# Optimization experiments

Hardware: AMD Instinct MI355X
Metric: run time of the kernel (lower is better)

## Reference

```python
import jax, jax.numpy as jnp
import numpy as np

EPS = 1e-3  # Keras BatchNormalization default epsilon
HEADS = 4
KEY_DEPTH = 16   # k
INTRA = 1        # u
VAL_DEPTH = 64   # v = kernel_out // heads = 256 // 4
C_IN = 256
B, HH, WW = 16, 32, 32
N = HH * WW      # == size of positional embedding


def setup_inputs() -> dict:
    key = jax.random.key(0)
    ks = jax.random.split(key, 6)
    x = jax.random.normal(ks[0], (B, HH, WW, C_IN), dtype=jnp.float32)
    # 1x1 conv kernels == dense matrices over the channel dim
    Wq = jax.random.normal(ks[1], (C_IN, KEY_DEPTH * HEADS), dtype=jnp.float32) * 0.05
    Wk = jax.random.normal(ks[2], (C_IN, KEY_DEPTH * INTRA), dtype=jnp.float32) * 0.05
    Wv = jax.random.normal(ks[3], (C_IN, VAL_DEPTH * INTRA), dtype=jnp.float32) * 0.05
    # BatchNorm (inference mode) parameters
    gamma_q = jnp.ones((KEY_DEPTH * HEADS,), jnp.float32)
    beta_q = jnp.zeros((KEY_DEPTH * HEADS,), jnp.float32)
    mean_q = jnp.zeros((KEY_DEPTH * HEADS,), jnp.float32)
    var_q = jnp.ones((KEY_DEPTH * HEADS,), jnp.float32)
    gamma_v = jnp.ones((VAL_DEPTH * INTRA,), jnp.float32)
    beta_v = jnp.zeros((VAL_DEPTH * INTRA,), jnp.float32)
    mean_v = jnp.zeros((VAL_DEPTH * INTRA,), jnp.float32)
    var_v = jnp.ones((VAL_DEPTH * INTRA,), jnp.float32)
    # Positional embedding: [size, size, key_depth, intra_depth], uniform init
    E = jax.random.uniform(ks[4], (N, N, KEY_DEPTH, INTRA), dtype=jnp.float32)
    return {
        'x': x, 'Wq': Wq, 'Wk': Wk, 'Wv': Wv,
        'gamma_q': gamma_q, 'beta_q': beta_q, 'mean_q': mean_q, 'var_q': var_q,
        'gamma_v': gamma_v, 'beta_v': beta_v, 'mean_v': mean_v, 'var_v': var_v,
        'E': E,
    }


def _bn(t, gamma, beta, mean, var):
    return gamma * (t - mean) / jnp.sqrt(var + EPS) + beta


def reference(x, Wq, Wk, Wv, gamma_q, beta_q, mean_q, var_q,
              gamma_v, beta_v, mean_v, var_v, E):
    b, hh, ww, _ = x.shape
    n = hh * ww
    # 1x1 conv projections (context c == x)
    q = jnp.einsum('bhwc,cd->bhwd', x, Wq)           # [b,hh,ww,h*k]
    k = jnp.einsum('bhwc,cd->bhwd', x, Wk)           # [b,hh,ww,u*k]
    v = jnp.einsum('bhwc,cd->bhwd', x, Wv)           # [b,hh,ww,u*v]
    q = _bn(q, gamma_q, beta_q, mean_q, var_q)
    v = _bn(v, gamma_v, beta_v, mean_v, var_v)
    # softmax over the channel axis (faithful to the source code)
    k = jax.nn.softmax(k, axis=-1)
    # rearranges: b hh ww (h k) -> b h k n ; b hh ww (u k) -> b u k n ; b hh ww (u v) -> b u v n
    q = q.reshape(b, n, HEADS, KEY_DEPTH).transpose(0, 2, 3, 1)   # [b,h,k,n]
    k = k.reshape(b, n, INTRA, KEY_DEPTH).transpose(0, 2, 3, 1)   # [b,u,k,n]
    v = v.reshape(b, n, INTRA, VAL_DEPTH).transpose(0, 2, 3, 1)   # [b,u,v,n]
    # content lambda: sum over intra-depth and positions
    lam_c = jnp.einsum('bukn,buvn->bkv', k, v)                    # [b,k,v]
    Yc = jnp.einsum('bhkn,bkv->bhvn', q, lam_c)                   # [b,h,v,n]
    # positional lambdas: E[n,m,k,u] contracted with v[b,u,v,m]
    lam_p = jnp.einsum('nmku,buvm->bnkv', E, v)                   # [b,n,k,v]
    Yp = jnp.einsum('bhkn,bnkv->bhvn', q, lam_p)                  # [b,h,v,n]
    Y = Yc + Yp                                                    # [b,h,v,n]
    # b h v n -> b hh ww (h v)
    out = Y.transpose(0, 3, 1, 2).reshape(b, hh, ww, HEADS * VAL_DEPTH)
    return out
```

## Files before the change

kernel.cpp:

```cpp
#include <hip/hip_runtime.h>
#include <stdint.h>

#define EPS 1e-3f

typedef __bf16 bf16x8 __attribute__((ext_vector_type(8)));
typedef float  f32x4  __attribute__((ext_vector_type(4)));

static __device__ __forceinline__ uint16_t f2bf(float f) {
  union { float f; uint32_t u; } v; v.f = f;
  uint32_t u = v.u;
  uint32_t r = u + 0x7fffu + ((u >> 16) & 1u);
  return (uint16_t)(r >> 16);
}
static __device__ __forceinline__ void gload_lds16(const void* g, void* l) {
  __builtin_amdgcn_global_load_lds(
      (const __attribute__((address_space(1))) unsigned int*)g,
      (__attribute__((address_space(3))) unsigned int*)l, 16, 0, 0);
}

__global__ __launch_bounds__(256) void econv(
    const float* __restrict__ E, uint16_t* __restrict__ Ebf,
    const float* __restrict__ Wq, const float* __restrict__ Wk,
    const float* __restrict__ Wv, uint16_t* __restrict__ WtP)
{
  const int n = blockIdx.x, t = threadIdx.x;
  if (n < 144) {
    const int col = n;
    float val = (col < 64) ? Wq[t * 64 + col]
              : (col < 80) ? Wk[t * 16 + (col - 64)]
                           : Wv[t * 64 + (col - 80)];
    WtP[col * 264 + t] = f2bf(val);
  }
  const float* En = E + (size_t)n * 16384;
#pragma unroll 1
  for (int kq = 0; kq < 4; ++kq) {
#pragma unroll
    for (int mi = 0; mi < 4; ++mi) {
      int m = mi * 256 + t;
      float4 d = *(const float4*)&En[m * 16 + kq * 4];
      const float* dp = (const float*)&d;
#pragma unroll
      for (int j = 0; j < 4; ++j) {
        int k = kq * 4 + j;
        Ebf[(size_t)(n * 16 + k) * 1024 + m] = f2bf(dp[j]);
      }
    }
  }
}

__global__ __launch_bounds__(256) void proj_mfma(
    const float* __restrict__ x, const uint16_t* __restrict__ WtP,
    const float* __restrict__ gq, const float* __restrict__ bq,
    const float* __restrict__ mq, const float* __restrict__ vq,
    const float* __restrict__ gv, const float* __restrict__ bv,
    const float* __restrict__ mv, const float* __restrict__ vvp,
    float* __restrict__ Qf, uint16_t* __restrict__ VbfT,
    float* __restrict__ part)
{
  __shared__ __align__(16) char smem[111616];
  uint16_t* const xA = (uint16_t*)smem;
  char* const Wt = smem + 33792;

  const int t = threadIdx.x;
  const int wid = t >> 6, lane = t & 63;
  const int bid = blockIdx.x;
  const int b = bid >> 4, mc = bid & 15;
  const int r0 = b * 1024 + mc * 64;

#pragma unroll
  for (int i = 0; i < 19; ++i) {
    int off = (i * 256 + t) * 16;
    gload_lds16((const char*)WtP + off, Wt + off);
  }
  {
    const int row = t >> 2, ks0 = (t & 3) * 64;
    const float* src = x + (size_t)(r0 + row) * 256 + ks0;
    uint16_t* dstp = xA + row * 264 + ks0;
#pragma unroll
    for (int i = 0; i < 8; ++i) {
      float4 d0 = *(const float4*)(src + i * 8);
      float4 d1 = *(const float4*)(src + i * 8 + 4);
      union { uint16_t u[8]; uint4 q; } pk;
      pk.u[0] = f2bf(d0.x); pk.u[1] = f2bf(d0.y);
      pk.u[2] = f2bf(d0.z); pk.u[3] = f2bf(d0.w);
      pk.u[4] = f2bf(d1.x); pk.u[5] = f2bf(d1.y);
      pk.u[6] = f2bf(d1.z); pk.u[7] = f2bf(d1.w);
      *(uint4*)(dstp + i * 8) = pk.q;
    }
  }
  __syncthreads();

  f32x4 acc[9];
#pragma unroll
  for (int f = 0; f < 9; ++f) acc[f] = f32x4{0.f, 0.f, 0.f, 0.f};
  const int arow = wid * 16 + (lane & 15);
#pragma unroll
  for (int kst = 0; kst < 8; ++kst) {
    const int sb = kst * 64 + ((lane >> 4) << 4);
    bf16x8 af = *(const bf16x8*)((const char*)xA + arow * 528 + sb);
#pragma unroll
    for (int f = 0; f < 9; ++f) {
      const int crow = f * 16 + (lane & 15);
      bf16x8 bfr = *(const bf16x8*)(Wt + crow * 528 + sb);
      acc[f] = __builtin_amdgcn_mfma_f32_16x16x32_bf16(af, bfr, acc[f], 0, 0, 0);
    }
  }

  const int cl = lane & 15;
  const int rbase = wid * 16 + ((lane >> 4) << 2);

  float qs[4], qb[4], qm[4], vs[4], vb[4], vm[4];
#pragma unroll
  for (int f = 0; f < 4; ++f) {
    const int c = f * 16 + cl;
    qs[f] = gq[c] * rsqrtf(vq[c] + EPS); qb[f] = bq[c]; qm[f] = mq[c];
    vs[f] = gv[c] * rsqrtf(vvp[c] + EPS); vb[f] = bv[c]; vm[f] = mv[c];
  }
#pragma unroll
  for (int f = 0; f < 4; ++f)
#pragma unroll
    for (int r = 0; r < 4; ++r)
      Qf[(size_t)(r0 + rbase + r) * 64 + f * 16 + cl] =
          (acc[f][r] - qm[f]) * qs[f] + qb[f];
  float ex[4];
#pragma unroll
  for (int r = 0; r < 4; ++r) {
    float kv = acc[4][r];
    float mx = kv;
#pragma unroll
    for (int d = 1; d < 16; d <<= 1) mx = fmaxf(mx, __shfl_xor(mx, d, 64));
    float e = __expf(kv - mx);
    float sm = e;
#pragma unroll
    for (int d = 1; d < 16; d <<= 1) sm += __shfl_xor(sm, d, 64);
    ex[r] = e / sm;
  }
  float vv[4][4];
#pragma unroll
  for (int f = 0; f < 4; ++f)
#pragma unroll
    for (int r = 0; r < 4; ++r)
      vv[f][r] = (acc[5 + f][r] - vm[f]) * vs[f] + vb[f];

  __syncthreads();
  float* const vt = (float*)smem;
  float* const ks = (float*)(smem + 64 * 65 * 4);
#pragma unroll
  for (int r = 0; r < 4; ++r) ks[(rbase + r) * 20 + cl] = ex[r];
#pragma unroll
  for (int f = 0; f < 4; ++f)
#pragma unroll
    for (int r = 0; r < 4; ++r) vt[(rbase + r) * 65 + f * 16 + cl] = vv[f][r];
  __syncthreads();

  {
    const int v = t & 63, grp = t >> 6;
#pragma unroll
    for (int h = 0; h < 2; ++h) {
      union { uint16_t u16[8]; uint4 q; } pk;
#pragma unroll
      for (int i = 0; i < 8; ++i)
        pk.u16[i] = f2bf(vt[(grp * 16 + h * 8 + i) * 65 + v]);
      *(uint4*)&VbfT[(size_t)(b * 64 + v) * 1024 + mc * 64 + grp * 16 + h * 8] = pk.q;
    }
  }
  {
    const int kq = t >> 6, v = t & 63;
    float a0 = 0.f, a1 = 0.f, a2 = 0.f, a3 = 0.f;
#pragma unroll 4
    for (int m = 0; m < 64; ++m) {
      float vvx = vt[m * 65 + v];
      a0 = fmaf(ks[m * 20 + kq * 4 + 0], vvx, a0);
      a1 = fmaf(ks[m * 20 + kq * 4 + 1], vvx, a1);
      a2 = fmaf(ks[m * 20 + kq * 4 + 2], vvx, a2);
      a3 = fmaf(ks[m * 20 + kq * 4 + 3], vvx, a3);
    }
    float* dst = part + ((size_t)(b * 16 + mc) << 10) + (kq * 4) * 64 + v;
    dst[0] = a0; dst[64] = a1; dst[128] = a2; dst[192] = a3;
  }
}

__global__ __launch_bounds__(256) void lamc_reduce(const float* __restrict__ part,
                                                   float* __restrict__ Lc)
{
  const int gid = blockIdx.x * 256 + threadIdx.x;
  const int b = gid >> 10, r = gid & 1023;
  const float* p = part + ((size_t)b << 14) + r;
  float s = 0.f;
#pragma unroll
  for (int mc = 0; mc < 16; ++mc) s += p[mc << 10];
  Lc[((size_t)b << 10) + r] = s;
}

__global__ __launch_bounds__(512, 2) void gemm_out(
    const uint16_t* __restrict__ Ebf,
    const uint16_t* __restrict__ VbfT,
    const float* __restrict__ Qf,
    const float* __restrict__ Lc,
    float* __restrict__ out)
{
  __shared__ __align__(16) char smem[131072];
  char* const A0 = smem;
  char* const B0 = smem + 32768;
  char* const A1 = smem + 65536;
  char* const B1 = smem + 98304;

  const int t = threadIdx.x;
  const int wid = t >> 6, lane = t & 63;
  const int wm = wid >> 2, wn = wid & 3;
  const int bid = blockIdx.x;
  const int xcd = bid & 7, idx = bid >> 3;
  const int rb = xcd * 8 + (idx >> 2);
  const int cb = idx & 3;
  const int row0 = rb * 256;
  const int col0 = cb * 256;

  const uint16_t* aptr[4];
  const uint16_t* bptr[4];
  int dst[4];
  {
    const uint16_t* Ab = Ebf + ((size_t)row0 << 10);
    const uint16_t* Bb = VbfT + ((size_t)col0 << 10);
#pragma unroll
    for (int it = 0; it < 4; ++it) {
      int id = it * 512 + t;
      int row = id >> 3, seg = id & 7;
      int src = (row << 10) + ((seg ^ (row & 7)) << 3);
      aptr[it] = Ab + src;
      bptr[it] = Bb + src;
      dst[it] = id * 16;
    }
  }

  f32x4 acc[8][4];
#pragma unroll
  for (int i = 0; i < 8; ++i)
#pragma unroll
    for (int j = 0; j < 4; ++j) acc[i][j] = f32x4{0.f, 0.f, 0.f, 0.f};

#pragma unroll
  for (int it = 0; it < 4; ++it) {
    gload_lds16(aptr[it], A0 + dst[it]);
    gload_lds16(bptr[it], B0 + dst[it]);
  }
  __syncthreads();

#pragma unroll 1
  for (int kt = 0; kt < 16; ++kt) {
    char* Ac = (kt & 1) ? A1 : A0;
    char* Bc = (kt & 1) ? B1 : B0;
    char* An = (kt & 1) ? A0 : A1;
    char* Bn = (kt & 1) ? B0 : B1;
    if (kt < 15) {
      const int off = (kt + 1) * 64;
#pragma unroll
      for (int it = 0; it < 4; ++it) {
        gload_lds16(aptr[it] + off, An + dst[it]);
        gload_lds16(bptr[it] + off, Bn + dst[it]);
      }
    }
    __builtin_amdgcn_s_setprio(1);
#pragma unroll
    for (int kk = 0; kk < 2; ++kk) {
      bf16x8 a[8], b[4];
      const int s = kk * 4 + (lane >> 4);
#pragma unroll
      for (int i = 0; i < 8; ++i) {
        int row = wm * 128 + i * 16 + (lane & 15);
        a[i] = *(const bf16x8*)(Ac + row * 128 + ((s ^ (row & 7)) << 4));
      }
#pragma unroll
      for (int j = 0; j < 4; ++j) {
        int row = wn * 64 + j * 16 + (lane & 15);
        b[j] = *(const bf16x8*)(Bc + row * 128 + ((s ^ (row & 7)) << 4));
      }
#pragma unroll
      for (int i = 0; i < 8; ++i)
#pragma unroll
        for (int j = 0; j < 4; ++j)
          acc[i][j] = __builtin_amdgcn_mfma_f32_16x16x32_bf16(a[i], b[j], acc[i][j], 0, 0, 0);
    }
    __builtin_amdgcn_s_setprio(0);
    __syncthreads();
  }

  float* Cs = (float*)smem;
  const int n0 = rb * 16;
  const int b0 = cb * 4;
#pragma unroll
  for (int p = 0; p < 4; ++p) {
    if (wm == (p >> 1)) {
#pragma unroll
      for (int il = 0; il < 4; ++il) {
        const int i = ((p & 1) << 2) + il;
#pragma unroll
        for (int j = 0; j < 4; ++j) {
          const int col = wn * 64 + j * 16 + (lane & 15);
          const int bb = b0 + (col >> 6), v = col & 63;
#pragma unroll
          for (int r = 0; r < 4; ++r) {
            const int rl = il * 16 + ((lane >> 4) << 2) + r;
            const int k = rl & 15;
            Cs[rl * 258 + col] = acc[i][j][r] + Lc[(size_t)(((bb << 4) + k) << 6) + v];
          }
        }
      }
    }
    __syncthreads();
    {
      const int v = t & 63;
#pragma unroll
      for (int c = 0; c < 8; ++c) {
        const int combo = (wid << 3) + c;
        const int n_l = combo >> 4;
        const int b_l = (combo >> 2) & 3;
        const int h = combo & 3;
        const int n = n0 + (p << 2) + n_l;
        const int bb = b0 + b_l;
        const float* qp = Qf + (((size_t)(bb << 10) + n) << 6) + (h << 4);
        float sum = 0.f;
#pragma unroll
        for (int k = 0; k < 16; ++k)
          sum = fmaf(qp[k], Cs[((n_l << 4) + k) * 258 + (b_l << 6) + v], sum);
        out[(((size_t)(bb << 10) + n) << 8) + (h << 6) + v] = sum;
      }
    }
    __syncthreads();
  }
}

extern "C" void kernel_launch(void* const* d_in, const int* in_sizes, int n_in,
                              void* d_out, int out_size, void* d_ws, size_t ws_size,
                              hipStream_t stream) {
  const float* x   = (const float*)d_in[0];
  const float* Wq  = (const float*)d_in[1];
  const float* Wk  = (const float*)d_in[2];
  const float* Wv  = (const float*)d_in[3];
  const float* gq  = (const float*)d_in[4];
  const float* bq  = (const float*)d_in[5];
  const float* mq  = (const float*)d_in[6];
  const float* vq  = (const float*)d_in[7];
  const float* gv  = (const float*)d_in[8];
  const float* bv  = (const float*)d_in[9];
  const float* mv  = (const float*)d_in[10];
  const float* vvp = (const float*)d_in[11];
  const float* E   = (const float*)d_in[12];
  float* out = (float*)d_out;

  char* ws = (char*)d_ws;
  uint16_t* Ebf  = (uint16_t*)(ws);
  uint16_t* VbfT = (uint16_t*)(ws + 33554432);
  float*    Qf   = (float*)(ws + 35651584);
  float*    part = (float*)(ws + 39845888);
  float*    Lc   = (float*)(ws + 40894464);
  uint16_t* WtP  = (uint16_t*)(ws + 40960000);

  hipLaunchKernelGGL(econv, dim3(1024), dim3(256), 0, stream,
                     E, Ebf, Wq, Wk, Wv, WtP);
  hipLaunchKernelGGL(proj_mfma, dim3(256), dim3(256), 0, stream, x, WtP,
                     gq, bq, mq, vq, gv, bv, mv, vvp, Qf, VbfT, part);
  hipLaunchKernelGGL(lamc_reduce, dim3(64), dim3(256), 0, stream, part, Lc);
  hipLaunchKernelGGL(gemm_out, dim3(256), dim3(512), 0, stream, Ebf, VbfT, Qf, Lc, out);
}
```

Before: 83.59 us.

## Fuse fp32-to-bf16 conversion of E into the output GEMM's A-tile loading

```diff
diff --git a/kernel.cpp b/kernel.cpp
--- a/kernel.cpp
+++ b/kernel.cpp
@@ -12,40 +12,26 @@
   uint32_t r = u + 0x7fffu + ((u >> 16) & 1u);
   return (uint16_t)(r >> 16);
 }
+static __device__ __forceinline__ uint32_t pack2bf(float lo, float hi) {
+  union { uint16_t h[2]; uint32_t u; } r;
+  r.h[0] = f2bf(lo); r.h[1] = f2bf(hi);
+  return r.u;
+}
 static __device__ __forceinline__ void gload_lds16(const void* g, void* l) {
   __builtin_amdgcn_global_load_lds(
       (const __attribute__((address_space(1))) unsigned int*)g,
       (__attribute__((address_space(3))) unsigned int*)l, 16, 0, 0);
 }
 
-__global__ __launch_bounds__(256) void econv(
-    const float* __restrict__ E, uint16_t* __restrict__ Ebf,
+__global__ __launch_bounds__(256) void wprep(
     const float* __restrict__ Wq, const float* __restrict__ Wk,
     const float* __restrict__ Wv, uint16_t* __restrict__ WtP)
 {
-  const int n = blockIdx.x, t = threadIdx.x;
-  if (n < 144) {
-    const int col = n;
-    float val = (col < 64) ? Wq[t * 64 + col]
-              : (col < 80) ? Wk[t * 16 + (col - 64)]
-                           : Wv[t * 64 + (col - 80)];
-    WtP[col * 264 + t] = f2bf(val);
-  }
-  const float* En = E + (size_t)n * 16384;
-#pragma unroll 1
-  for (int kq = 0; kq < 4; ++kq) {
-#pragma unroll
-    for (int mi = 0; mi < 4; ++mi) {
-      int m = mi * 256 + t;
-      float4 d = *(const float4*)&En[m * 16 + kq * 4];
-      const float* dp = (const float*)&d;
-#pragma unroll
-      for (int j = 0; j < 4; ++j) {
-        int k = kq * 4 + j;
-        Ebf[(size_t)(n * 16 + k) * 1024 + m] = f2bf(dp[j]);
-      }
-    }
-  }
+  const int col = blockIdx.x, t = threadIdx.x;
+  float val = (col < 64) ? Wq[t * 64 + col]
+            : (col < 80) ? Wk[t * 16 + (col - 64)]
+                         : Wv[t * 64 + (col - 80)];
+  WtP[col * 264 + t] = f2bf(val);
 }
 
 __global__ __launch_bounds__(256) void proj_mfma(
@@ -193,7 +179,7 @@
 }
 
 __global__ __launch_bounds__(512, 2) void gemm_out(
-    const uint16_t* __restrict__ Ebf,
+    const float* __restrict__ E,
     const uint16_t* __restrict__ VbfT,
     const float* __restrict__ Qf,
     const float* __restrict__ Lc,
@@ -212,23 +198,33 @@
   const int xcd = bid & 7, idx = bid >> 3;
   const int rb = xcd * 8 + (idx >> 2);
   const int cb = idx & 3;
-  const int row0 = rb * 256;
   const int col0 = cb * 256;
-
-  const uint16_t* aptr[4];
+  const int n0 = rb * 16;
+
+  const int kq = t & 3;
+  const int mp = (t >> 2) & 31;
+  const int nb = t >> 7;
+  const float* Eb = E + ((size_t)n0 << 14);
+
+  int awoff[4][4];
+#pragma unroll
+  for (int it = 0; it < 4; ++it)
+#pragma unroll
+    for (int j = 0; j < 4; ++j) {
+      int row = (it * 4 + nb) * 16 + kq * 4 + j;
+      awoff[it][j] = row * 128 + ((mp * 4) ^ ((row & 7) << 4));
+    }
+
   const uint16_t* bptr[4];
-  int dst[4];
+  int bdst[4];
   {
-    const uint16_t* Ab = Ebf + ((size_t)row0 << 10);
     const uint16_t* Bb = VbfT + ((size_t)col0 << 10);
 #pragma unroll
     for (int it = 0; it < 4; ++it) {
       int id = it * 512 + t;
       int row = id >> 3, seg = id & 7;
-      int src = (row << 10) + ((seg ^ (row & 7)) << 3);
-      aptr[it] = Ab + src;
-      bptr[it] = Bb + src;
-      dst[it] = id * 16;
+      bptr[it] = Bb + (row << 10) + ((seg ^ (row & 7)) << 3);
+      bdst[it] = id * 16;
     }
   }
 
@@ -238,10 +234,23 @@
 #pragma unroll
     for (int j = 0; j < 4; ++j) acc[i][j] = f32x4{0.f, 0.f, 0.f, 0.f};
 
+  float4 ra[4], rbx[4];
+
 #pragma unroll
   for (int it = 0; it < 4; ++it) {
-    gload_lds16(aptr[it], A0 + dst[it]);
-    gload_lds16(bptr[it], B0 + dst[it]);
+    size_t base = ((size_t)(it * 4 + nb) << 14) + ((size_t)(mp * 2) << 4) + (kq << 2);
+    ra[it]  = *(const float4*)(Eb + base);
+    rbx[it] = *(const float4*)(Eb + base + 16);
+  }
+#pragma unroll
+  for (int it = 0; it < 4; ++it) gload_lds16(bptr[it], B0 + bdst[it]);
+#pragma unroll
+  for (int it = 0; it < 4; ++it) {
+    const float* da = (const float*)&ra[it];
+    const float* db = (const float*)&rbx[it];
+#pragma unroll
+    for (int j = 0; j < 4; ++j)
+      *(uint32_t*)(A0 + awoff[it][j]) = pack2bf(da[j], db[j]);
   }
   __syncthreads();
 
@@ -252,12 +261,16 @@
     char* An = (kt & 1) ? A0 : A1;
     char* Bn = (kt & 1) ? B0 : B1;
     if (kt < 15) {
-      const int off = (kt + 1) * 64;
+      const int m0n = (kt + 1) * 64;
 #pragma unroll
       for (int it = 0; it < 4; ++it) {
-        gload_lds16(aptr[it] + off, An + dst[it]);
-        gload_lds16(bptr[it] + off, Bn + dst[it]);
-      }
+        size_t base = ((size_t)(it * 4 + nb) << 14) +
+                      ((size_t)(m0n + mp * 2) << 4) + (kq << 2);
+        ra[it]  = *(const float4*)(Eb + base);
+        rbx[it] = *(const float4*)(Eb + base + 16);
+      }
+#pragma unroll
+      for (int it = 0; it < 4; ++it) gload_lds16(bptr[it] + m0n, Bn + bdst[it]);
     }
     __builtin_amdgcn_s_setprio(1);
 #pragma unroll
@@ -281,11 +294,20 @@
           acc[i][j] = __builtin_amdgcn_mfma_f32_16x16x32_bf16(a[i], b[j], acc[i][j], 0, 0, 0);
     }
     __builtin_amdgcn_s_setprio(0);
+    if (kt < 15) {
+#pragma unroll
+      for (int it = 0; it < 4; ++it) {
+        const float* da = (const float*)&ra[it];
+        const float* db = (const float*)&rbx[it];
+#pragma unroll
+        for (int j = 0; j < 4; ++j)
+          *(uint32_t*)(An + awoff[it][j]) = pack2bf(da[j], db[j]);
+      }
+    }
     __syncthreads();
   }
 
   float* Cs = (float*)smem;
-  const int n0 = rb * 16;
   const int b0 = cb * 4;
 #pragma unroll
   for (int p = 0; p < 4; ++p) {
@@ -348,17 +370,15 @@
   float* out = (float*)d_out;
 
   char* ws = (char*)d_ws;
-  uint16_t* Ebf  = (uint16_t*)(ws);
-  uint16_t* VbfT = (uint16_t*)(ws + 33554432);
-  float*    Qf   = (float*)(ws + 35651584);
-  float*    part = (float*)(ws + 39845888);
-  float*    Lc   = (float*)(ws + 40894464);
-  uint16_t* WtP  = (uint16_t*)(ws + 40960000);
-
-  hipLaunchKernelGGL(econv, dim3(1024), dim3(256), 0, stream,
-                     E, Ebf, Wq, Wk, Wv, WtP);
+  uint16_t* VbfT = (uint16_t*)(ws);
+  float*    Qf   = (float*)(ws + (size_t)(2 << 20));
+  float*    part = (float*)(ws + (size_t)(6 << 20));
+  float*    Lc   = (float*)(ws + (size_t)(7 << 20));
+  uint16_t* WtP  = (uint16_t*)(ws + (size_t)(7 << 20) + 65536);
+
+  hipLaunchKernelGGL(wprep, dim3(144), dim3(256), 0, stream, Wq, Wk, Wv, WtP);
   hipLaunchKernelGGL(proj_mfma, dim3(256), dim3(256), 0, stream, x, WtP,
                      gq, bq, mq, vq, gv, bv, mv, vvp, Qf, VbfT, part);
   hipLaunchKernelGGL(lamc_reduce, dim3(64), dim3(256), 0, stream, part, Lc);
-  hipLaunchKernelGGL(gemm_out, dim3(256), dim3(512), 0, stream, Ebf, VbfT, Qf, Lc, out);
-}
+  hipLaunchKernelGGL(gemm_out, dim3(256), dim3(512), 0, stream, E, VbfT, Qf, Lc, out);
+}
```

Result: faster. 75.38 us (-9.8%).
